# Kernel tuning notes

Measured on AMD Instinct MI355X. Metric: run time of the kernel, lower is better.

## Reference

```python
import jax, jax.numpy as jnp
import numpy as np

B, T, H, S = 64, 512, 768, 128  # batch, seq_len, hidden_size, num_statements


def setup_inputs() -> dict:
    key = jax.random.key(0)
    ks = jax.random.split(key, 6)
    hidden = jax.random.normal(ks[0], (B, T, H), dtype=jnp.float32)
    # per-token statement ids, sorted (statements appear contiguously in source order)
    statements_ids = jnp.sort(jax.random.randint(ks[1], (B, T), 0, S), axis=-1).astype(jnp.int32)
    scale = 1.0 / np.sqrt(H)
    w1 = jax.random.normal(ks[2], (H, H), dtype=jnp.float32) * scale
    b1 = jnp.zeros((H,), dtype=jnp.float32)
    w2 = jax.random.normal(ks[3], (H, H), dtype=jnp.float32) * scale
    b2 = jnp.zeros((H,), dtype=jnp.float32)
    w3 = jax.random.normal(ks[4], (H, 1), dtype=jnp.float32) * scale
    b3 = jnp.zeros((1,), dtype=jnp.float32)
    return {"hidden": hidden, "statements_ids": statements_ids,
            "w1": w1, "b1": b1, "w2": w2, "b2": b2, "w3": w3, "b3": b3}


def _segment_mean(x, sid):
    # x: [T, H], sid: [T] -> [S, H] mean of tokens per statement id
    sums = jax.ops.segment_sum(x, sid, num_segments=S)            # [S, H]
    cnts = jax.ops.segment_sum(jnp.ones((x.shape[0],), x.dtype), sid, num_segments=S)  # [S]
    return sums / jnp.maximum(cnts, 1.0)[:, None]


def reference(hidden, statements_ids, w1, b1, w2, b2, w3, b3):
    # per-statement mean pooling (scatter-mean), vectorized over batch
    pooled = jax.vmap(_segment_mean)(hidden, statements_ids)      # [B, S, H]
    # CodeCoverageMLP: fc1 -> GELU -> fc2 -> GELU -> fc3 -> sigmoid (dropout = eval identity)
    x = jax.nn.gelu(pooled @ w1 + b1, approximate=False)
    x = jax.nn.gelu(x @ w2 + b2, approximate=False)
    preds = jax.nn.sigmoid(x @ w3 + b3)                           # [B, S, 1]
    return preds[..., 0]                                          # [B, S]
```

## Files before the change

### kernel.cpp

```cpp
#include <hip/hip_runtime.h>
#include <stdint.h>

#define NB 64
#define NT 512
#define NH 768
#define NS 128
#define NM (NB*NS)

typedef _Float16 half8 __attribute__((ext_vector_type(8)));
typedef _Float16 half4 __attribute__((ext_vector_type(4)));
typedef __attribute__((ext_vector_type(4))) float f32x4;

__device__ __forceinline__ float gelu_exact(float x) {
  return 0.5f * x * (1.0f + erff(x * 0.70710678118654752440f));
}

__device__ __forceinline__ void gll16(const void* g, void* l) {
  __builtin_amdgcn_global_load_lds(
      (__attribute__((address_space(1))) unsigned int*)g,
      (__attribute__((address_space(3))) unsigned int*)l,
      16, 0, 0);
}

__global__ void prep_w_kernel(const float* __restrict__ w1, const float* __restrict__ w2,
                              _Float16* __restrict__ W) {
  int id = blockIdx.x * 256 + threadIdx.x;
  int n  = id % NH;
  int t  = id / NH;
  int kc = t % 96;
  int w  = t / 96;
  const float* src = w ? w2 : w1;
  int k0 = kc * 8;
  half8 h;
#pragma unroll
  for (int i = 0; i < 8; ++i)
    h[i] = (_Float16)src[(size_t)(k0 + i) * NH + n];
  *(half8*)&W[(size_t)w * NH * NH + (size_t)n * NH + (size_t)(k0 ^ ((n & 7) << 3))] = h;
}

__global__ __launch_bounds__(256)
void pool_kernel(const float* __restrict__ hidden, const int* __restrict__ sid,
                 _Float16* __restrict__ Ahi, _Float16* __restrict__ Alo) {
  __shared__ int   s_sid[NT];
  __shared__ short s_e0[NS + 1];
  const int b = blockIdx.y, cc = blockIdx.x;
  const int tid = threadIdx.x;
  for (int t = tid; t < NT; t += 256) s_sid[t] = sid[b * NT + t];
  __syncthreads();
  for (int t = tid; t < NT; t += 256) {
    const int cur  = s_sid[t];
    const int prev = t ? s_sid[t - 1] : -1;
    for (int s = prev + 1; s <= cur; ++s) s_e0[s] = (short)t;
    if (t == NT - 1)
      for (int s = cur + 1; s <= NS; ++s) s_e0[s] = (short)NT;
  }
  __syncthreads();

  const int c4  = tid & 15;
  const int sg  = tid >> 4;
  const int col = cc * 64 + c4 * 4;
  const float* hb = hidden + (size_t)b * NT * NH;

  for (int s = sg; s < NS; s += 16) {
    const int e0 = s_e0[s], e1 = s_e0[s + 1];
    f32x4 acc = {0.f, 0.f, 0.f, 0.f};
    for (int t = e0; t < e1; ++t)
      acc += *(const f32x4*)(hb + (size_t)t * NH + col);
    const float inv = 1.0f / (float)((e1 > e0) ? (e1 - e0) : 1);
    const int m = b * NS + s;
    half4 h, l;
#pragma unroll
    for (int j = 0; j < 4; ++j) {
      float x = acc[j] * inv;
      h[j] = (_Float16)x;
      l[j] = (_Float16)(x - (float)h[j]);
    }
    const size_t off = (size_t)m * NH + (size_t)(col ^ ((m & 7) << 3));
    *(half4*)&Ahi[off] = h;
    *(half4*)&Alo[off] = l;
  }
}

__global__ void finish_kernel(const float* __restrict__ part, const float* __restrict__ b3,
                              float* __restrict__ out) {
  int i = blockIdx.x * 256 + threadIdx.x;
  float s = b3[0];
#pragma unroll
  for (int j = 0; j < 12; ++j) s += part[(size_t)j * NM + i];
  out[i] = 1.0f / (1.0f + expf(-s));
}

template <int EPI>
__global__ __launch_bounds__(256, 3)
void gemm_kernel(const _Float16* __restrict__ Ahi, const _Float16* __restrict__ Alo,
                 const _Float16* __restrict__ W, const float* __restrict__ bias,
                 _Float16* __restrict__ Chi, _Float16* __restrict__ Clo,
                 const float* __restrict__ w3, float* __restrict__ part) {
  __shared__ _Float16 lds[16384];

  const int tid  = threadIdx.x;
  const int lane = tid & 63;
  const int wave = tid >> 6;
  const int wr = wave >> 1, wc = wave & 1;

  const int bid = blockIdx.x;
  const int idp = (bid & 7) * 96 + (bid >> 3);
  const int mb = idp / 6, nb = idp % 6;
  const int row0 = mb * 64, col0 = nb * 128;

  const int lr = lane & 15, lk = lane >> 4;
  const int sr = lane >> 3;
  const int scol = (lane & 7) * 8;

  f32x4 acc[2][4] = {};

  for (int kt = 0; kt < NH / 64; ++kt) {
    const int kb = kt * 64;
#pragma unroll
    for (int i = 0; i < 8; ++i) {
      const int cid = i * 4 + wave;
      if (cid < 16) {
        const int arr = cid >> 3;
        const int r = (cid & 7) * 8 + sr;
        const size_t g = (size_t)(row0 + r) * NH + kb + scol;
        gll16((arr ? Alo : Ahi) + g, &lds[arr * 4096 + (cid & 7) * 512]);
      } else {
        const int r = (cid - 16) * 8 + sr;
        gll16(W + (size_t)(col0 + r) * NH + kb + scol, &lds[8192 + (cid - 16) * 512]);
      }
    }
    __syncthreads();

#pragma unroll
    for (int kk = 0; kk < 2; ++kk) {
      const int kl = kk * 32 + lk * 8;
      half8 ah[2], al[2], bw[4];
#pragma unroll
      for (int mf = 0; mf < 2; ++mf) {
        const int ar = wr * 32 + mf * 16 + lr;
        const int ad = ar * 64 + (kl ^ ((ar & 7) << 3));
        ah[mf] = *(const half8*)&lds[ad];
        al[mf] = *(const half8*)&lds[4096 + ad];
      }
#pragma unroll
      for (int nf = 0; nf < 4; ++nf) {
        const int br = wc * 64 + nf * 16 + lr;
        bw[nf] = *(const half8*)&lds[8192 + br * 64 + (kl ^ ((br & 7) << 3))];
      }
#pragma unroll
      for (int mf = 0; mf < 2; ++mf)
#pragma unroll
        for (int nf = 0; nf < 4; ++nf) {
          acc[mf][nf] = __builtin_amdgcn_mfma_f32_16x16x32_f16(ah[mf], bw[nf], acc[mf][nf], 0, 0, 0);
          acc[mf][nf] = __builtin_amdgcn_mfma_f32_16x16x32_f16(al[mf], bw[nf], acc[mf][nf], 0, 0, 0);
        }
    }
    __syncthreads();
  }

  if (EPI == 0) {
#pragma unroll
    for (int nf = 0; nf < 4; ++nf) {
      const int col = col0 + wc * 64 + nf * 16 + lr;
      const float bv = bias[col];
#pragma unroll
      for (int mf = 0; mf < 2; ++mf) {
#pragma unroll
        for (int r = 0; r < 4; ++r) {
          const int rowm = row0 + wr * 32 + mf * 16 + lk * 4 + r;
          float g = gelu_exact(acc[mf][nf][r] + bv);
          _Float16 h = (_Float16)g;
          _Float16 l = (_Float16)(g - (float)h);
          size_t off = (size_t)rowm * NH + (size_t)(col ^ ((rowm & 7) << 3));
          Chi[off] = h;
          Clo[off] = l;
        }
      }
    }
  } else {
    float bv[4], wv[4];
#pragma unroll
    for (int nf = 0; nf < 4; ++nf) {
      const int col = col0 + wc * 64 + nf * 16 + lr;
      bv[nf] = bias[col];
      wv[nf] = w3[col];
    }
#pragma unroll
    for (int mf = 0; mf < 2; ++mf) {
#pragma unroll
      for (int r = 0; r < 4; ++r) {
        float p = 0.f;
#pragma unroll
        for (int nf = 0; nf < 4; ++nf)
          p += gelu_exact(acc[mf][nf][r] + bv[nf]) * wv[nf];
        p += __shfl_xor(p, 1, 16);
        p += __shfl_xor(p, 2, 16);
        p += __shfl_xor(p, 4, 16);
        p += __shfl_xor(p, 8, 16);
        if (lr == 0) {
          const int rowm = row0 + wr * 32 + mf * 16 + lk * 4 + r;
          part[((size_t)(nb * 2 + wc)) * NM + rowm] = p;
        }
      }
    }
  }
}

extern "C" void kernel_launch(void* const* d_in, const int* in_sizes, int n_in,
                              void* d_out, int out_size, void* d_ws, size_t ws_size,
                              hipStream_t stream) {
  (void)in_sizes; (void)n_in; (void)out_size; (void)ws_size;
  const float* hidden = (const float*)d_in[0];
  const int*   sid    = (const int*)d_in[1];
  const float* w1     = (const float*)d_in[2];
  const float* b1     = (const float*)d_in[3];
  const float* w2     = (const float*)d_in[4];
  const float* b2     = (const float*)d_in[5];
  const float* w3     = (const float*)d_in[6];
  const float* b3     = (const float*)d_in[7];
  float* out = (float*)d_out;

  char* p = (char*)d_ws;
  const size_t actE = (size_t)NM * NH;
  _Float16* Ahi  = (_Float16*)p; p += actE * 2;
  _Float16* Alo  = (_Float16*)p; p += actE * 2;
  _Float16* X1hi = (_Float16*)p; p += actE * 2;
  _Float16* X1lo = (_Float16*)p; p += actE * 2;
  _Float16* W    = (_Float16*)p; p += (size_t)2 * NH * NH * 2;
  float*    part = (float*)p;    p += (size_t)12 * NM * 4;

  prep_w_kernel<<<2 * 96 * NH / 256, 256, 0, stream>>>(w1, w2, W);
  pool_kernel<<<dim3(12, NB), 256, 0, stream>>>(hidden, sid, Ahi, Alo);

  gemm_kernel<0><<<768, 256, 0, stream>>>(Ahi, Alo, W, b1, X1hi, X1lo, nullptr, nullptr);
  gemm_kernel<1><<<768, 256, 0, stream>>>(X1hi, X1lo, W + (size_t)NH * NH, b2,
                                          nullptr, nullptr, w3, part);
  finish_kernel<<<NM / 256, 256, 0, stream>>>(part, b3, out);
}
```

Before: 242.4 us.

## Load weight fragments directly into registers and halve GEMM row tile

```diff
diff --git a/kernel.cpp b/kernel.cpp
--- a/kernel.cpp
+++ b/kernel.cpp
@@ -35,7 +35,7 @@
 #pragma unroll
   for (int i = 0; i < 8; ++i)
     h[i] = (_Float16)src[(size_t)(k0 + i) * NH + n];
-  *(half8*)&W[(size_t)w * NH * NH + (size_t)n * NH + (size_t)(k0 ^ ((n & 7) << 3))] = h;
+  *(half8*)&W[(size_t)w * NH * NH + (size_t)n * NH + k0] = h;
 }
 
 __global__ __launch_bounds__(256)
@@ -75,7 +75,7 @@
       h[j] = (_Float16)x;
       l[j] = (_Float16)(x - (float)h[j]);
     }
-    const size_t off = (size_t)m * NH + (size_t)(col ^ ((m & 7) << 3));
+    const size_t off = (size_t)m * NH + col;
     *(half4*)&Ahi[off] = h;
     *(half4*)&Alo[off] = l;
   }
@@ -91,12 +91,12 @@
 }
 
 template <int EPI>
-__global__ __launch_bounds__(256, 3)
+__global__ __launch_bounds__(256, 4)
 void gemm_kernel(const _Float16* __restrict__ Ahi, const _Float16* __restrict__ Alo,
-                 const _Float16* __restrict__ W, const float* __restrict__ bias,
+                 const _Float16* __restrict__ Wg, const float* __restrict__ bias,
                  _Float16* __restrict__ Chi, _Float16* __restrict__ Clo,
                  const float* __restrict__ w3, float* __restrict__ part) {
-  __shared__ _Float16 lds[16384];
+  __shared__ _Float16 lds[8192];
 
   const int tid  = threadIdx.x;
   const int lane = tid & 63;
@@ -104,56 +104,52 @@
   const int wr = wave >> 1, wc = wave & 1;
 
   const int bid = blockIdx.x;
-  const int idp = (bid & 7) * 96 + (bid >> 3);
+  const int idp = (bid & 7) * 192 + (bid >> 3);
   const int mb = idp / 6, nb = idp % 6;
-  const int row0 = mb * 64, col0 = nb * 128;
-
-  const int lr = lane & 15, lk = lane >> 4;
-  const int sr = lane >> 3;
-  const int scol = (lane & 7) * 8;
-
-  f32x4 acc[2][4] = {};
-
-  for (int kt = 0; kt < NH / 64; ++kt) {
-    const int kb = kt * 64;
-#pragma unroll
-    for (int i = 0; i < 8; ++i) {
-      const int cid = i * 4 + wave;
-      if (cid < 16) {
-        const int arr = cid >> 3;
-        const int r = (cid & 7) * 8 + sr;
-        const size_t g = (size_t)(row0 + r) * NH + kb + scol;
-        gll16((arr ? Alo : Ahi) + g, &lds[arr * 4096 + (cid & 7) * 512]);
-      } else {
-        const int r = (cid - 16) * 8 + sr;
-        gll16(W + (size_t)(col0 + r) * NH + kb + scol, &lds[8192 + (cid - 16) * 512]);
+  const int row0 = mb * 32, col0 = nb * 128;
+
+  const int lr  = lane & 15;
+  const int lk4 = lane >> 4;
+  const int lcol = lr * 8;
+
+  const _Float16* wrow[4];
+#pragma unroll
+  for (int nf = 0; nf < 4; ++nf)
+    wrow[nf] = Wg + (size_t)(col0 + wc * 64 + nf * 16 + lr) * NH + lk4 * 8;
+
+  f32x4 acc[4] = {};
+
+  for (int kt = 0; kt < NH / 128; ++kt) {
+    const int kb = kt * 128;
+
+    half8 bw[4][4];
+#pragma unroll
+    for (int kk = 0; kk < 4; ++kk)
+#pragma unroll
+      for (int nf = 0; nf < 4; ++nf)
+        bw[kk][nf] = *(const half8*)(wrow[nf] + kb + kk * 32);
+
+#pragma unroll
+    for (int i = 0; i < 2; ++i) {
+      const int chunk = i * 4 + wave;
+      const int r = chunk * 4 + lk4;
+      const size_t src = (size_t)(row0 + r) * NH + kb + (lcol ^ ((r & 7) << 3));
+      gll16(Ahi + src, &lds[chunk * 512]);
+      gll16(Alo + src, &lds[4096 + chunk * 512]);
+    }
+    __syncthreads();
+
+#pragma unroll
+    for (int kk = 0; kk < 4; ++kk) {
+      const int ar = wr * 16 + lr;
+      const int ad = ar * 128 + ((kk * 32 + lk4 * 8) ^ ((ar & 7) << 3));
+      half8 ah = *(const half8*)&lds[ad];
+      half8 al = *(const half8*)&lds[4096 + ad];
+#pragma unroll
+      for (int nf = 0; nf < 4; ++nf) {
+        acc[nf] = __builtin_amdgcn_mfma_f32_16x16x32_f16(ah, bw[kk][nf], acc[nf], 0, 0, 0);
+        acc[nf] = __builtin_amdgcn_mfma_f32_16x16x32_f16(al, bw[kk][nf], acc[nf], 0, 0, 0);
       }
-    }
-    __syncthreads();
-
-#pragma unroll
-    for (int kk = 0; kk < 2; ++kk) {
-      const int kl = kk * 32 + lk * 8;
-      half8 ah[2], al[2], bw[4];
-#pragma unroll
-      for (int mf = 0; mf < 2; ++mf) {
-        const int ar = wr * 32 + mf * 16 + lr;
-        const int ad = ar * 64 + (kl ^ ((ar & 7) << 3));
-        ah[mf] = *(const half8*)&lds[ad];
-        al[mf] = *(const half8*)&lds[4096 + ad];
-      }
-#pragma unroll
-      for (int nf = 0; nf < 4; ++nf) {
-        const int br = wc * 64 + nf * 16 + lr;
-        bw[nf] = *(const half8*)&lds[8192 + br * 64 + (kl ^ ((br & 7) << 3))];
-      }
-#pragma unroll
-      for (int mf = 0; mf < 2; ++mf)
-#pragma unroll
-        for (int nf = 0; nf < 4; ++nf) {
-          acc[mf][nf] = __builtin_amdgcn_mfma_f32_16x16x32_f16(ah[mf], bw[nf], acc[mf][nf], 0, 0, 0);
-          acc[mf][nf] = __builtin_amdgcn_mfma_f32_16x16x32_f16(al[mf], bw[nf], acc[mf][nf], 0, 0, 0);
-        }
     }
     __syncthreads();
   }
@@ -164,17 +160,14 @@
       const int col = col0 + wc * 64 + nf * 16 + lr;
       const float bv = bias[col];
 #pragma unroll
-      for (int mf = 0; mf < 2; ++mf) {
-#pragma unroll
-        for (int r = 0; r < 4; ++r) {
-          const int rowm = row0 + wr * 32 + mf * 16 + lk * 4 + r;
-          float g = gelu_exact(acc[mf][nf][r] + bv);
-          _Float16 h = (_Float16)g;
-          _Float16 l = (_Float16)(g - (float)h);
-          size_t off = (size_t)rowm * NH + (size_t)(col ^ ((rowm & 7) << 3));
-          Chi[off] = h;
-          Clo[off] = l;
-        }
+      for (int r = 0; r < 4; ++r) {
+        const int rowm = row0 + wr * 16 + lk4 * 4 + r;
+        float g = gelu_exact(acc[nf][r] + bv);
+        _Float16 h = (_Float16)g;
+        _Float16 l = (_Float16)(g - (float)h);
+        const size_t off = (size_t)rowm * NH + col;
+        Chi[off] = h;
+        Clo[off] = l;
       }
     }
   } else {
@@ -186,21 +179,18 @@
       wv[nf] = w3[col];
     }
 #pragma unroll
-    for (int mf = 0; mf < 2; ++mf) {
-#pragma unroll
-      for (int r = 0; r < 4; ++r) {
-        float p = 0.f;
-#pragma unroll
-        for (int nf = 0; nf < 4; ++nf)
-          p += gelu_exact(acc[mf][nf][r] + bv[nf]) * wv[nf];
-        p += __shfl_xor(p, 1, 16);
-        p += __shfl_xor(p, 2, 16);
-        p += __shfl_xor(p, 4, 16);
-        p += __shfl_xor(p, 8, 16);
-        if (lr == 0) {
-          const int rowm = row0 + wr * 32 + mf * 16 + lk * 4 + r;
-          part[((size_t)(nb * 2 + wc)) * NM + rowm] = p;
-        }
+    for (int r = 0; r < 4; ++r) {
+      float p = 0.f;
+#pragma unroll
+      for (int nf = 0; nf < 4; ++nf)
+        p += gelu_exact(acc[nf][r] + bv[nf]) * wv[nf];
+      p += __shfl_xor(p, 1, 16);
+      p += __shfl_xor(p, 2, 16);
+      p += __shfl_xor(p, 4, 16);
+      p += __shfl_xor(p, 8, 16);
+      if (lr == 0) {
+        const int rowm = row0 + wr * 16 + lk4 * 4 + r;
+        part[((size_t)(nb * 2 + wc)) * NM + rowm] = p;
       }
     }
   }
@@ -232,8 +222,8 @@
   prep_w_kernel<<<2 * 96 * NH / 256, 256, 0, stream>>>(w1, w2, W);
   pool_kernel<<<dim3(12, NB), 256, 0, stream>>>(hidden, sid, Ahi, Alo);
 
-  gemm_kernel<0><<<768, 256, 0, stream>>>(Ahi, Alo, W, b1, X1hi, X1lo, nullptr, nullptr);
-  gemm_kernel<1><<<768, 256, 0, stream>>>(X1hi, X1lo, W + (size_t)NH * NH, b2,
-                                          nullptr, nullptr, w3, part);
+  gemm_kernel<0><<<1536, 256, 0, stream>>>(Ahi, Alo, W, b1, X1hi, X1lo, nullptr, nullptr);
+  gemm_kernel<1><<<1536, 256, 0, stream>>>(X1hi, X1lo, W + (size_t)NH * NH, b2,
+                                           nullptr, nullptr, w3, part);
   finish_kernel<<<NM / 256, 256, 0, stream>>>(part, b3, out);
 }
```

New measurement: 333.1 us. 37.4% more time.
